# Optimization experiments

Hardware: AMD Instinct MI355X
Metric: run time of the kernel (lower is better)

## Reference

```python
import jax, jax.numpy as jnp
import numpy as np

N_NODES = 500_000
N_EDGES = 16_000_000


def setup_inputs() -> dict:
    key = jax.random.key(0)
    k1, k2, k3, k4 = jax.random.split(key, 4)
    x = jax.random.normal(k1, (N_NODES, 1), dtype=jnp.float32)
    edge_index = jax.random.randint(k2, (2, N_EDGES), 0, N_NODES, dtype=jnp.int64)
    W1 = jax.random.normal(k3, (1, 8), dtype=jnp.float32) * (1.0 / np.sqrt(1))
    b1 = jnp.zeros((8,), dtype=jnp.float32)
    W2 = jax.random.normal(k4, (8, 2), dtype=jnp.float32) * (1.0 / np.sqrt(8))
    b2 = jnp.zeros((2,), dtype=jnp.float32)
    return {"x": x, "edge_index": edge_index, "W1": W1, "b1": b1, "W2": W2, "b2": b2}


def _gcn_conv(x, src, dst, norm, W, b):
    # PyG GCNConv: h = X W; out_i = sum_{(j->i)} norm_ji * h_j + b
    h = x @ W                         # [N, out]
    msg = h[src] * norm[:, None]      # [E', out] gather + scale
    out = jax.ops.segment_sum(msg, dst, num_segments=N_NODES)  # scatter-add
    return out + b


def reference(x, edge_index, W1, b1, W2, b2):
    # add self-loops (PyG default add_self_loops=True)
    loop = jnp.arange(N_NODES, dtype=edge_index.dtype)
    src = jnp.concatenate([edge_index[0], loop])
    dst = jnp.concatenate([edge_index[1], loop])
    # symmetric normalization: deg^{-1/2}[src] * deg^{-1/2}[dst]
    deg = jax.ops.segment_sum(jnp.ones_like(dst, dtype=x.dtype), dst, num_segments=N_NODES)
    dis = jnp.where(deg > 0, jax.lax.rsqrt(deg), 0.0)
    norm = dis[src] * dis[dst]        # [E']
    h = jax.nn.relu(_gcn_conv(x, src, dst, norm, W1, b1))
    return _gcn_conv(h, src, dst, norm, W2, b2)
```

## Files before the change

kernel.cpp:

```cpp
#include <hip/hip_runtime.h>

#define N_NODES 500000
typedef unsigned int u32;
typedef unsigned short u16;

#define NPB    1024
#define NBUCK  ((N_NODES + NPB - 1) / NPB)
#define CAP    40960
#define CH     8192
#define TB     1024
#define SRCMASK 0x3FFFFFu

typedef int  v4i __attribute__((ext_vector_type(4)));
typedef unsigned int v4u __attribute__((ext_vector_type(4)));
__device__ inline int  nt1i(const int* p) { return __builtin_nontemporal_load(p); }
__device__ inline u32  nt1u(const u32* p) { return __builtin_nontemporal_load(p); }
__device__ inline v4u  nt4u(const u32* p) { return __builtin_nontemporal_load((const v4u*)p); }

__global__ __launch_bounds__(TB) void k_scatter_fused(
        const int* __restrict__ src, const int* __restrict__ dst, int E,
        u32* __restrict__ cur_g, u32* __restrict__ rec) {
    __shared__ u32 srec[CH];
    __shared__ u16 sbk[CH];
    __shared__ u32 hist[NBUCK];
    __shared__ u32 sc[512];
    __shared__ u32 scn_ex[NBUCK];
    __shared__ u32 cur2[NBUCK];
    __shared__ u32 gbase[NBUCK];
    int tid = threadIdx.x, bid = blockIdx.x;
    for (int b = tid; b < NBUCK; b += TB) hist[b] = 0;
    __syncthreads();
    int e0 = bid * CH, e1 = min(E, e0 + CH), n = e1 - e0;
    for (int e = e0 + tid; e < e1; e += TB)
        atomicAdd(&hist[((u32)nt1i(dst + e)) >> 10], 1u);
    __syncthreads();
    if (tid < 512) sc[tid] = (tid < NBUCK) ? hist[tid] : 0u;
    __syncthreads();
    for (int off = 1; off < 512; off <<= 1) {
        u32 t = 0;
        if (tid < 512 && tid >= off) t = sc[tid - off];
        __syncthreads();
        if (tid < 512) sc[tid] += t;
        __syncthreads();
    }
    if (tid < NBUCK) {
        u32 ex = sc[tid] - hist[tid];
        scn_ex[tid] = ex;
        cur2[tid] = ex;
        gbase[tid] = hist[tid] ? atomicAdd(&cur_g[tid], hist[tid]) : 0u;
    }
    __syncthreads();
    for (int e = e0 + tid; e < e1; e += TB) {
        u32 d = (u32)nt1i(dst + e);
        u32 s = (u32)nt1i(src + e);
        u32 b = d >> 10;
        u32 p = atomicAdd(&cur2[b], 1u);
        srec[p] = ((d & (NPB - 1u)) << 22) | s;
        sbk[p] = (u16)b;
    }
    __syncthreads();
    for (int p = tid; p < n; p += TB) {
        u32 b = sbk[p];
        u32 slot = gbase[b] + ((u32)p - scn_ex[b]);
        rec[(size_t)b * CAP + slot] = srec[p];
    }
}

__global__ __launch_bounds__(TB) void k_deg_dis(
        const u32* __restrict__ rec, const u32* __restrict__ cnt_g,
        const float* __restrict__ x,
        float* __restrict__ dis, float* __restrict__ m1) {
    __shared__ u32 cnt[NPB];
    int tid = threadIdx.x, bid = blockIdx.x;
    for (int l = tid; l < NPB; l += TB) cnt[l] = 0;
    __syncthreads();
    const u32* r0 = rec + (size_t)bid * CAP;
    u32 n = cnt_g[bid];
    u32 nv = n >> 2;
    for (u32 i = tid; i < nv; i += TB) {
        v4u r = nt4u(r0 + (i << 2));
        atomicAdd(&cnt[r.x >> 22], 1u);
        atomicAdd(&cnt[r.y >> 22], 1u);
        atomicAdd(&cnt[r.z >> 22], 1u);
        atomicAdd(&cnt[r.w >> 22], 1u);
    }
    for (u32 e = (nv << 2) + tid; e < n; e += TB)
        atomicAdd(&cnt[nt1u(r0 + e) >> 22], 1u);
    __syncthreads();
    int node0 = bid << 10;
    int nn = min(NPB, N_NODES - node0);
    for (int l = tid; l < nn; l += TB) {
        int node = node0 + l;
        float r = rsqrtf((float)(cnt[l] + 1u));
        dis[node] = r;
        m1[node] = r * x[node];
    }
}

__global__ __launch_bounds__(TB) void k_layer1(
        const u32* __restrict__ rec, const u32* __restrict__ cnt_g,
        const float* __restrict__ dis, const float* __restrict__ m1,
        const float* __restrict__ W1, const float* __restrict__ b1,
        const float* __restrict__ W2, const float* __restrict__ b2,
        float2* __restrict__ h2m, float2* __restrict__ out) {
    __shared__ float acc[NPB];
    int tid = threadIdx.x, bid = blockIdx.x;
    for (int l = tid; l < NPB; l += TB) acc[l] = 0.f;
    __syncthreads();
    const u32* r0 = rec + (size_t)bid * CAP;
    u32 n = cnt_g[bid];
    u32 nv = n >> 2;
    for (u32 i = tid; i < nv; i += TB) {
        v4u r = nt4u(r0 + (i << 2));
        float v0 = m1[r.x & SRCMASK];
        float v1 = m1[r.y & SRCMASK];
        float v2 = m1[r.z & SRCMASK];
        float v3 = m1[r.w & SRCMASK];
        atomicAdd(&acc[r.x >> 22], v0);
        atomicAdd(&acc[r.y >> 22], v1);
        atomicAdd(&acc[r.z >> 22], v2);
        atomicAdd(&acc[r.w >> 22], v3);
    }
    for (u32 e = (nv << 2) + tid; e < n; e += TB) {
        u32 r = nt1u(r0 + e);
        atomicAdd(&acc[r >> 22], m1[r & SRCMASK]);
    }
    __syncthreads();
    int node0 = bid << 10;
    int nn = min(NPB, N_NODES - node0);
    for (int l = tid; l < nn; l += TB) {
        int node = node0 + l;
        float d = dis[node];
        float s = d * (acc[l] + m1[node]);
        float a0 = 0.f, a1 = 0.f;
#pragma unroll
        for (int k = 0; k < 8; ++k) {
            float h = fmaxf(W1[k] * s + b1[k], 0.f);
            a0 += h * W2[2 * k + 0];
            a1 += h * W2[2 * k + 1];
        }
        h2m[node] = make_float2(d * a0, d * a1);
        out[node] = make_float2(b2[0] + d * d * a0, b2[1] + d * d * a1);
    }
}

__global__ __launch_bounds__(TB) void k_layer2(
        const u32* __restrict__ rec, const u32* __restrict__ cnt_g,
        const float* __restrict__ dis, const float2* __restrict__ h2m,
        float2* __restrict__ out) {
    __shared__ float ax[NPB];
    __shared__ float ay[NPB];
    int tid = threadIdx.x, bid = blockIdx.x;
    for (int l = tid; l < NPB; l += TB) { ax[l] = 0.f; ay[l] = 0.f; }
    __syncthreads();
    const u32* r0 = rec + (size_t)bid * CAP;
    u32 n = cnt_g[bid];
    u32 nv = n >> 2;
    for (u32 i = tid; i < nv; i += TB) {
        v4u r = nt4u(r0 + (i << 2));
        float2 v0 = h2m[r.x & SRCMASK];
        float2 v1 = h2m[r.y & SRCMASK];
        float2 v2 = h2m[r.z & SRCMASK];
        float2 v3 = h2m[r.w & SRCMASK];
        atomicAdd(&ax[r.x >> 22], v0.x);
        atomicAdd(&ay[r.x >> 22], v0.y);
        atomicAdd(&ax[r.y >> 22], v1.x);
        atomicAdd(&ay[r.y >> 22], v1.y);
        atomicAdd(&ax[r.z >> 22], v2.x);
        atomicAdd(&ay[r.z >> 22], v2.y);
        atomicAdd(&ax[r.w >> 22], v3.x);
        atomicAdd(&ay[r.w >> 22], v3.y);
    }
    for (u32 e = (nv << 2) + tid; e < n; e += TB) {
        u32 r = nt1u(r0 + e);
        float2 v = h2m[r & SRCMASK];
        atomicAdd(&ax[r >> 22], v.x);
        atomicAdd(&ay[r >> 22], v.y);
    }
    __syncthreads();
    int node0 = bid << 10;
    int nn = min(NPB, N_NODES - node0);
    for (int l = tid; l < nn; l += TB) {
        int node = node0 + l;
        float d = dis[node];
        float2 o = out[node];
        out[node] = make_float2(o.x + d * ax[l], o.y + d * ay[l]);
    }
}

__global__ void f_count_deg(const int* __restrict__ dst, int E,
                            u32* __restrict__ deg) {
    int i = blockIdx.x * blockDim.x + threadIdx.x;
    int stride = gridDim.x * blockDim.x;
    for (int e = i; e < E; e += stride) atomicAdd(&deg[dst[e]], 1u);
}
__global__ void f_dis_sinit(const u32* __restrict__ deg, const float* __restrict__ x,
                            float* __restrict__ dis, float* __restrict__ s, int N) {
    int i = blockIdx.x * blockDim.x + threadIdx.x;
    if (i < N) {
        float r = rsqrtf((float)(deg[i] + 1u));
        dis[i] = r;
        s[i] = r * r * x[i];
    }
}
__global__ void f_agg1(const int* __restrict__ src, const int* __restrict__ dst,
                       int E, const float* __restrict__ dis,
                       const float* __restrict__ x, float* __restrict__ s) {
    int i = blockIdx.x * blockDim.x + threadIdx.x;
    int stride = gridDim.x * blockDim.x;
    for (int e = i; e < E; e += stride) {
        int sj = src[e], dj = dst[e];
        atomicAdd(&s[dj], dis[sj] * dis[dj] * x[sj]);
    }
}
__global__ void f_node2(const float* __restrict__ s, const float* __restrict__ dis,
                        const float* __restrict__ W1, const float* __restrict__ b1,
                        const float* __restrict__ W2, const float* __restrict__ b2,
                        float2* __restrict__ h2, float2* __restrict__ out, int N) {
    int i = blockIdx.x * blockDim.x + threadIdx.x;
    if (i >= N) return;
    float si = s[i];
    float a0 = 0.f, a1 = 0.f;
#pragma unroll
    for (int k = 0; k < 8; ++k) {
        float hk = fmaxf(W1[k] * si + b1[k], 0.f);
        a0 += hk * W2[2 * k + 0];
        a1 += hk * W2[2 * k + 1];
    }
    h2[i] = make_float2(a0, a1);
    float r2 = dis[i] * dis[i];
    out[i] = make_float2(b2[0] + r2 * a0, b2[1] + r2 * a1);
}
__global__ void f_agg2(const int* __restrict__ src, const int* __restrict__ dst,
                       int E, const float* __restrict__ dis,
                       const float2* __restrict__ h2, float* __restrict__ out) {
    int i = blockIdx.x * blockDim.x + threadIdx.x;
    int stride = gridDim.x * blockDim.x;
    for (int e = i; e < E; e += stride) {
        int sj = src[e], dj = dst[e];
        float nm = dis[sj] * dis[dj];
        float2 v = h2[sj];
        atomicAdd(&out[2 * dj + 0], nm * v.x);
        atomicAdd(&out[2 * dj + 1], nm * v.y);
    }
}

extern "C" void kernel_launch(void* const* d_in, const int* in_sizes, int n_in,
                              void* d_out, int out_size, void* d_ws, size_t ws_size,
                              hipStream_t stream) {
    const float* x  = (const float*)d_in[0];
    const int*   ei = (const int*)d_in[1];
    const float* W1 = (const float*)d_in[2];
    const float* b1 = (const float*)d_in[3];
    const float* W2 = (const float*)d_in[4];
    const float* b2 = (const float*)d_in[5];

    const int N = N_NODES;
    const int E = in_sizes[1] / 2;
    const int* src = ei;
    const int* dst = ei + E;
    float* out = (float*)d_out;
    char* ws = (char*)d_ws;

    size_t off = 0;
    auto take = [&](size_t bytes) { size_t o = off; off = (off + bytes + 255) & ~(size_t)255; return o; };
    size_t off_cur  = take(NBUCK * 4);
    size_t off_dis  = take((size_t)N * 4);
    size_t off_m1   = take((size_t)N * 4);
    size_t off_h2m  = take((size_t)N * 8);
    size_t off_rec  = take((size_t)NBUCK * CAP * 4 + 16);
    size_t need     = off;

    if (ws_size >= need) {
        u32* cur_g  = (u32*)(ws + off_cur);
        float* dis  = (float*)(ws + off_dis);
        float* m1   = (float*)(ws + off_m1);
        float2* h2m = (float2*)(ws + off_h2m);
        u32* rec    = (u32*)(ws + off_rec);

        hipMemsetAsync(cur_g, 0, NBUCK * 4, stream);
        const int nchunks = (E + CH - 1) / CH;
        k_scatter_fused<<<nchunks, TB, 0, stream>>>(src, dst, E, cur_g, rec);
        k_deg_dis      <<<NBUCK,   TB, 0, stream>>>(rec, cur_g, x, dis, m1);
        k_layer1       <<<NBUCK,   TB, 0, stream>>>(rec, cur_g, dis, m1,
                                                    W1, b1, W2, b2,
                                                    h2m, (float2*)out);
        k_layer2       <<<NBUCK,   TB, 0, stream>>>(rec, cur_g, dis, h2m,
                                                    (float2*)out);
        return;
    }

    u32* deg   = (u32*)(ws);
    float* dis = (float*)(ws + (size_t)N * 4);
    float* s   = (float*)(ws + (size_t)N * 8);
    float2* h2 = (float2*)(ws + (size_t)N * 12);
    hipMemsetAsync(deg, 0, (size_t)N * 4, stream);
    int nodeBlocks = (N + 255) / 256;
    int edgeBlocks = (E + 255) / 256;
    f_count_deg<<<edgeBlocks, 256, 0, stream>>>(dst, E, deg);
    f_dis_sinit<<<nodeBlocks, 256, 0, stream>>>(deg, x, dis, s, N);
    f_agg1     <<<edgeBlocks, 256, 0, stream>>>(src, dst, E, dis, x, s);
    f_node2    <<<nodeBlocks, 256, 0, stream>>>(s, dis, W1, b1, W2, b2, h2,
                                                (float2*)out, N);
    f_agg2     <<<edgeBlocks, 256, 0, stream>>>(src, dst, E, dis, h2, out);
}
```

Before: 526.9 us.

## Halve node buckets to 512 and cache edge loads in registers during scatter

Bucket size drops from 1024 to 512 nodes, which doubles the bucket count to about 977, halves per-bucket capacity, and repacks records as a 10-bit local node index plus a 19-bit source. The aggregation kernels now launch 512-thread blocks over twice as many buckets, giving finer parallelism and smaller shared accumulators. The scatter kernel keeps each thread's dst/src values in registers (8 per thread) rather than reading them from global memory twice, and widens the prefix scan to 1024 entries. The risks are more scattered global writes from the scatter pass and a higher chance of overflowing the smaller per-bucket capacity on skewed inputs.

```diff
diff --git a/kernel.cpp b/kernel.cpp
--- a/kernel.cpp
+++ b/kernel.cpp
@@ -4,43 +4,51 @@
 typedef unsigned int u32;
 typedef unsigned short u16;
 
-#define NPB    1024
+#define NPB    512
 #define NBUCK  ((N_NODES + NPB - 1) / NPB)
-#define CAP    40960
+#define CAP    20480
 #define CH     8192
-#define TB     1024
-#define SRCMASK 0x3FFFFFu
-
-typedef int  v4i __attribute__((ext_vector_type(4)));
+#define EPT    8
+#define STB    1024
+#define LTB    512
+#define SRC19  0x7FFFFu
+
 typedef unsigned int v4u __attribute__((ext_vector_type(4)));
 __device__ inline int  nt1i(const int* p) { return __builtin_nontemporal_load(p); }
 __device__ inline u32  nt1u(const u32* p) { return __builtin_nontemporal_load(p); }
 __device__ inline v4u  nt4u(const u32* p) { return __builtin_nontemporal_load((const v4u*)p); }
 
-__global__ __launch_bounds__(TB) void k_scatter_fused(
+__global__ __launch_bounds__(STB) void k_scatter_fused(
         const int* __restrict__ src, const int* __restrict__ dst, int E,
         u32* __restrict__ cur_g, u32* __restrict__ rec) {
     __shared__ u32 srec[CH];
     __shared__ u16 sbk[CH];
     __shared__ u32 hist[NBUCK];
-    __shared__ u32 sc[512];
+    __shared__ u32 sc[1024];
     __shared__ u32 scn_ex[NBUCK];
     __shared__ u32 cur2[NBUCK];
     __shared__ u32 gbase[NBUCK];
     int tid = threadIdx.x, bid = blockIdx.x;
-    for (int b = tid; b < NBUCK; b += TB) hist[b] = 0;
+    for (int b = tid; b < NBUCK; b += STB) hist[b] = 0;
     __syncthreads();
     int e0 = bid * CH, e1 = min(E, e0 + CH), n = e1 - e0;
-    for (int e = e0 + tid; e < e1; e += TB)
-        atomicAdd(&hist[((u32)nt1i(dst + e)) >> 10], 1u);
-    __syncthreads();
-    if (tid < 512) sc[tid] = (tid < NBUCK) ? hist[tid] : 0u;
-    __syncthreads();
-    for (int off = 1; off < 512; off <<= 1) {
-        u32 t = 0;
-        if (tid < 512 && tid >= off) t = sc[tid - off];
+    u32 dv[EPT], sv[EPT];
+#pragma unroll
+    for (int k = 0; k < EPT; ++k) {
+        int e = e0 + (k << 10) + tid;
+        if (e < e1) {
+            dv[k] = (u32)nt1i(dst + e);
+            sv[k] = (u32)nt1i(src + e);
+            atomicAdd(&hist[dv[k] >> 9], 1u);
+        }
+    }
+    __syncthreads();
+    sc[tid] = (tid < NBUCK) ? hist[tid] : 0u;
+    __syncthreads();
+    for (int off = 1; off < 1024; off <<= 1) {
+        u32 t = (tid >= off) ? sc[tid - off] : 0u;
         __syncthreads();
-        if (tid < 512) sc[tid] += t;
+        sc[tid] += t;
         __syncthreads();
     }
     if (tid < NBUCK) {
@@ -50,46 +58,48 @@
         gbase[tid] = hist[tid] ? atomicAdd(&cur_g[tid], hist[tid]) : 0u;
     }
     __syncthreads();
-    for (int e = e0 + tid; e < e1; e += TB) {
-        u32 d = (u32)nt1i(dst + e);
-        u32 s = (u32)nt1i(src + e);
-        u32 b = d >> 10;
-        u32 p = atomicAdd(&cur2[b], 1u);
-        srec[p] = ((d & (NPB - 1u)) << 22) | s;
-        sbk[p] = (u16)b;
-    }
-    __syncthreads();
-    for (int p = tid; p < n; p += TB) {
+#pragma unroll
+    for (int k = 0; k < EPT; ++k) {
+        int e = e0 + (k << 10) + tid;
+        if (e < e1) {
+            u32 b = dv[k] >> 9;
+            u32 p = atomicAdd(&cur2[b], 1u);
+            srec[p] = ((dv[k] & (NPB - 1u)) << 19) | sv[k];
+            sbk[p] = (u16)b;
+        }
+    }
+    __syncthreads();
+    for (int p = tid; p < n; p += STB) {
         u32 b = sbk[p];
         u32 slot = gbase[b] + ((u32)p - scn_ex[b]);
         rec[(size_t)b * CAP + slot] = srec[p];
     }
 }
 
-__global__ __launch_bounds__(TB) void k_deg_dis(
+__global__ __launch_bounds__(LTB) void k_deg_dis(
         const u32* __restrict__ rec, const u32* __restrict__ cnt_g,
         const float* __restrict__ x,
         float* __restrict__ dis, float* __restrict__ m1) {
     __shared__ u32 cnt[NPB];
     int tid = threadIdx.x, bid = blockIdx.x;
-    for (int l = tid; l < NPB; l += TB) cnt[l] = 0;
+    for (int l = tid; l < NPB; l += LTB) cnt[l] = 0;
     __syncthreads();
     const u32* r0 = rec + (size_t)bid * CAP;
     u32 n = cnt_g[bid];
     u32 nv = n >> 2;
-    for (u32 i = tid; i < nv; i += TB) {
+    for (u32 i = tid; i < nv; i += LTB) {
         v4u r = nt4u(r0 + (i << 2));
-        atomicAdd(&cnt[r.x >> 22], 1u);
-        atomicAdd(&cnt[r.y >> 22], 1u);
-        atomicAdd(&cnt[r.z >> 22], 1u);
-        atomicAdd(&cnt[r.w >> 22], 1u);
-    }
-    for (u32 e = (nv << 2) + tid; e < n; e += TB)
-        atomicAdd(&cnt[nt1u(r0 + e) >> 22], 1u);
-    __syncthreads();
-    int node0 = bid << 10;
+        atomicAdd(&cnt[r.x >> 19], 1u);
+        atomicAdd(&cnt[r.y >> 19], 1u);
+        atomicAdd(&cnt[r.z >> 19], 1u);
+        atomicAdd(&cnt[r.w >> 19], 1u);
+    }
+    for (u32 e = (nv << 2) + tid; e < n; e += LTB)
+        atomicAdd(&cnt[nt1u(r0 + e) >> 19], 1u);
+    __syncthreads();
+    int node0 = bid << 9;
     int nn = min(NPB, N_NODES - node0);
-    for (int l = tid; l < nn; l += TB) {
+    for (int l = tid; l < nn; l += LTB) {
         int node = node0 + l;
         float r = rsqrtf((float)(cnt[l] + 1u));
         dis[node] = r;
@@ -97,7 +107,7 @@
     }
 }
 
-__global__ __launch_bounds__(TB) void k_layer1(
+__global__ __launch_bounds__(LTB) void k_layer1(
         const u32* __restrict__ rec, const u32* __restrict__ cnt_g,
         const float* __restrict__ dis, const float* __restrict__ m1,
         const float* __restrict__ W1, const float* __restrict__ b1,
@@ -105,30 +115,30 @@
         float2* __restrict__ h2m, float2* __restrict__ out) {
     __shared__ float acc[NPB];
     int tid = threadIdx.x, bid = blockIdx.x;
-    for (int l = tid; l < NPB; l += TB) acc[l] = 0.f;
+    for (int l = tid; l < NPB; l += LTB) acc[l] = 0.f;
     __syncthreads();
     const u32* r0 = rec + (size_t)bid * CAP;
     u32 n = cnt_g[bid];
     u32 nv = n >> 2;
-    for (u32 i = tid; i < nv; i += TB) {
+    for (u32 i = tid; i < nv; i += LTB) {
         v4u r = nt4u(r0 + (i << 2));
-        float v0 = m1[r.x & SRCMASK];
-        float v1 = m1[r.y & SRCMASK];
-        float v2 = m1[r.z & SRCMASK];
-        float v3 = m1[r.w & SRCMASK];
-        atomicAdd(&acc[r.x >> 22], v0);
-        atomicAdd(&acc[r.y >> 22], v1);
-        atomicAdd(&acc[r.z >> 22], v2);
-        atomicAdd(&acc[r.w >> 22], v3);
-    }
-    for (u32 e = (nv << 2) + tid; e < n; e += TB) {
+        float v0 = m1[r.x & SRC19];
+        float v1 = m1[r.y & SRC19];
+        float v2 = m1[r.z & SRC19];
+        float v3 = m1[r.w & SRC19];
+        atomicAdd(&acc[r.x >> 19], v0);
+        atomicAdd(&acc[r.y >> 19], v1);
+        atomicAdd(&acc[r.z >> 19], v2);
+        atomicAdd(&acc[r.w >> 19], v3);
+    }
+    for (u32 e = (nv << 2) + tid; e < n; e += LTB) {
         u32 r = nt1u(r0 + e);
-        atomicAdd(&acc[r >> 22], m1[r & SRCMASK]);
-    }
-    __syncthreads();
-    int node0 = bid << 10;
+        atomicAdd(&acc[r >> 19], m1[r & SRC19]);
+    }
+    __syncthreads();
+    int node0 = bid << 9;
     int nn = min(NPB, N_NODES - node0);
-    for (int l = tid; l < nn; l += TB) {
+    for (int l = tid; l < nn; l += LTB) {
         int node = node0 + l;
         float d = dis[node];
         float s = d * (acc[l] + m1[node]);
@@ -144,43 +154,43 @@
     }
 }
 
-__global__ __launch_bounds__(TB) void k_layer2(
+__global__ __launch_bounds__(LTB) void k_layer2(
         const u32* __restrict__ rec, const u32* __restrict__ cnt_g,
         const float* __restrict__ dis, const float2* __restrict__ h2m,
         float2* __restrict__ out) {
     __shared__ float ax[NPB];
     __shared__ float ay[NPB];
     int tid = threadIdx.x, bid = blockIdx.x;
-    for (int l = tid; l < NPB; l += TB) { ax[l] = 0.f; ay[l] = 0.f; }
+    for (int l = tid; l < NPB; l += LTB) { ax[l] = 0.f; ay[l] = 0.f; }
     __syncthreads();
     const u32* r0 = rec + (size_t)bid * CAP;
     u32 n = cnt_g[bid];
     u32 nv = n >> 2;
-    for (u32 i = tid; i < nv; i += TB) {
+    for (u32 i = tid; i < nv; i += LTB) {
         v4u r = nt4u(r0 + (i << 2));
-        float2 v0 = h2m[r.x & SRCMASK];
-        float2 v1 = h2m[r.y & SRCMASK];
-        float2 v2 = h2m[r.z & SRCMASK];
-        float2 v3 = h2m[r.w & SRCMASK];
-        atomicAdd(&ax[r.x >> 22], v0.x);
-        atomicAdd(&ay[r.x >> 22], v0.y);
-        atomicAdd(&ax[r.y >> 22], v1.x);
-        atomicAdd(&ay[r.y >> 22], v1.y);
-        atomicAdd(&ax[r.z >> 22], v2.x);
-        atomicAdd(&ay[r.z >> 22], v2.y);
-        atomicAdd(&ax[r.w >> 22], v3.x);
-        atomicAdd(&ay[r.w >> 22], v3.y);
-    }
-    for (u32 e = (nv << 2) + tid; e < n; e += TB) {
+        float2 v0 = h2m[r.x & SRC19];
+        float2 v1 = h2m[r.y & SRC19];
+        float2 v2 = h2m[r.z & SRC19];
+        float2 v3 = h2m[r.w & SRC19];
+        atomicAdd(&ax[r.x >> 19], v0.x);
+        atomicAdd(&ay[r.x >> 19], v0.y);
+        atomicAdd(&ax[r.y >> 19], v1.x);
+        atomicAdd(&ay[r.y >> 19], v1.y);
+        atomicAdd(&ax[r.z >> 19], v2.x);
+        atomicAdd(&ay[r.z >> 19], v2.y);
+        atomicAdd(&ax[r.w >> 19], v3.x);
+        atomicAdd(&ay[r.w >> 19], v3.y);
+    }
+    for (u32 e = (nv << 2) + tid; e < n; e += LTB) {
         u32 r = nt1u(r0 + e);
-        float2 v = h2m[r & SRCMASK];
-        atomicAdd(&ax[r >> 22], v.x);
-        atomicAdd(&ay[r >> 22], v.y);
-    }
-    __syncthreads();
-    int node0 = bid << 10;
+        float2 v = h2m[r & SRC19];
+        atomicAdd(&ax[r >> 19], v.x);
+        atomicAdd(&ay[r >> 19], v.y);
+    }
+    __syncthreads();
+    int node0 = bid << 9;
     int nn = min(NPB, N_NODES - node0);
-    for (int l = tid; l < nn; l += TB) {
+    for (int l = tid; l < nn; l += LTB) {
         int node = node0 + l;
         float d = dis[node];
         float2 o = out[node];
@@ -280,20 +290,20 @@
 
         hipMemsetAsync(cur_g, 0, NBUCK * 4, stream);
         const int nchunks = (E + CH - 1) / CH;
-        k_scatter_fused<<<nchunks, TB, 0, stream>>>(src, dst, E, cur_g, rec);
-        k_deg_dis      <<<NBUCK,   TB, 0, stream>>>(rec, cur_g, x, dis, m1);
-        k_layer1       <<<NBUCK,   TB, 0, stream>>>(rec, cur_g, dis, m1,
-                                                    W1, b1, W2, b2,
-                                                    h2m, (float2*)out);
-        k_layer2       <<<NBUCK,   TB, 0, stream>>>(rec, cur_g, dis, h2m,
-                                                    (float2*)out);
+        k_scatter_fused<<<nchunks, STB, 0, stream>>>(src, dst, E, cur_g, rec);
+        k_deg_dis      <<<NBUCK,   LTB, 0, stream>>>(rec, cur_g, x, dis, m1);
+        k_layer1       <<<NBUCK,   LTB, 0, stream>>>(rec, cur_g, dis, m1,
+                                                     W1, b1, W2, b2,
+                                                     h2m, (float2*)out);
+        k_layer2       <<<NBUCK,   LTB, 0, stream>>>(rec, cur_g, dis, h2m,
+                                                     (float2*)out);
         return;
     }
 
-    u32* deg   = (u32*)(ws);
-    float* dis = (float*)(ws + (size_t)N * 4);
-    float* s   = (float*)(ws + (size_t)N * 8);
-    float2* h2 = (float2*)(ws + (size_t)N * 12);
+    u32* deg    = (u32*)(ws);
+    float* dis  = (float*)(ws + (size_t)N * 4);
+    float* s    = (float*)(ws + (size_t)N * 8);
+    float2* h2  = (float2*)(ws + (size_t)N * 12);
     hipMemsetAsync(deg, 0, (size_t)N * 4, stream);
     int nodeBlocks = (N + 255) / 256;
     int edgeBlocks = (E + 255) / 256;
```

Result: no change. 521.2 us (-1.1%).
